# Optimization experiments

Measured on AMD Instinct MI355X. Metric: run time of the kernel, lower is better.

The kernel has to match this reference:

```python
import jax, jax.numpy as jnp
import numpy as np
from jax import lax

BETA = 10.0  # undeclared global softmax temperature in the source
STRIDE = 1
PADDING = 1


def setup_inputs() -> dict:
    key = jax.random.key(0)
    k1, k2 = jax.random.split(key)
    B, Ci, Co, K, L = 32, 256, 256, 3, 7  # num_level_conv=8 -> L=7
    x = jax.random.normal(k1, (B, Ci, 56, 56), dtype=jnp.float32)
    p_c = jax.random.normal(k2, (Co, Ci, K, K, L), dtype=jnp.float32)
    # reset_parameters with num_level=8, s=1: t1=4, t2=floor(log2(1))=0,
    # t3=arange(-2,1)=[-2,-1,0] -> q_level = sort(-2**t3) ++ [0] ++ 2**t3
    t3 = np.arange(-2, 1, dtype=np.float32)
    q_level = jnp.asarray(
        np.concatenate([np.sort(-(2.0 ** t3)), np.zeros(1, np.float32), 2.0 ** t3]),
        dtype=jnp.float32,
    )
    return {"x": x, "p_c": p_c, "q_level": q_level}


def reference(x, p_c, q_level):
    # soft quantization of the conv weight
    norm = jnp.sqrt(jnp.sum(p_c * p_c, axis=-1, keepdims=True))  # (O,I,K,K,1)
    s_c = jax.nn.softmax(BETA * (p_c / norm), axis=-1)           # (O,I,K,K,L)
    conv_w = jnp.einsum("oihwl,l->oihw", s_c, q_level)           # (O,I,K,K)
    # the source's double loop over (kh,kw) with strided slicing + matmul
    # is exactly stride-S cross-correlation with zero padding
    out = lax.conv_general_dilated(
        x,
        conv_w,
        window_strides=(STRIDE, STRIDE),
        padding=[(PADDING, PADDING), (PADDING, PADDING)],
        dimension_numbers=("NCHW", "OIHW", "NCHW"),
    )
    return out
```

## Files before the change

kernel.cpp:

```cpp
#include <hip/hip_runtime.h>
#include <math.h>

#define CI   256
#define CO   256
#define HW   56
#define LQ   7
#define BETA 10.0f

typedef __attribute__((ext_vector_type(8))) short short8;
typedef __attribute__((ext_vector_type(4))) float f32x4;

__device__ __forceinline__ ushort f2bf(float f) {
    uint u = __float_as_uint(f);
    u += 0x7FFF + ((u >> 16) & 1);
    return (ushort)(u >> 16);
}

__global__ void quant_weights(const float* __restrict__ p_c,
                              const float* __restrict__ q_level,
                              short* __restrict__ W2) {
    int idx = blockIdx.x * blockDim.x + threadIdx.x;
    if (idx >= CO * CI) return;
    int co = idx >> 8, ci = idx & 255;
    float ql[LQ];
#pragma unroll
    for (int l = 0; l < LQ; ++l) ql[l] = q_level[l];
    const float* p = p_c + (size_t)idx * 9 * LQ;
#pragma unroll
    for (int t = 0; t < 9; ++t) {
        float pv[LQ];
        float ss = 0.f;
#pragma unroll
        for (int l = 0; l < LQ; ++l) { pv[l] = p[t * LQ + l]; ss += pv[l] * pv[l]; }
        float inv = rsqrtf(ss) * BETA;
        float m = -1e30f;
#pragma unroll
        for (int l = 0; l < LQ; ++l) { pv[l] *= inv; m = fmaxf(m, pv[l]); }
        float den = 0.f, num = 0.f;
#pragma unroll
        for (int l = 0; l < LQ; ++l) {
            float e = expf(pv[l] - m);
            den += e;
            num += e * ql[l];
        }
        float val = num / den;
        int widx = ((((ci >> 5) * 9 + t) * 4 + ((ci >> 3) & 3)) * 2048) + co * 8 + (ci & 7);
        W2[widx] = (short)f2bf(val);
    }
}

__global__ void prep_border(ushort* __restrict__ xt) {
    int idx = blockIdx.x * 256 + threadIdx.x;
    int b = blockIdx.y;
    if (idx >= 228 * 32) return;
    int pos = idx >> 5, chk = idx & 31;
    int hh, ww;
    if (pos < 58)       { hh = 0;  ww = pos; }
    else if (pos < 116) { hh = 57; ww = pos - 58; }
    else { int q = pos - 116; hh = 1 + (q >> 1); ww = (q & 1) ? 57 : 0; }
    size_t o = (((size_t)b * 58 + hh) * 58 + ww) * 256 + chk * 8;
    uint4 z = {0, 0, 0, 0};
    *(uint4*)&xt[o] = z;
}

__global__ __launch_bounds__(256) void prep_main(const float* __restrict__ x,
                                                 ushort* __restrict__ xt) {
    __shared__ ushort ld[256 * 60];
    const int tid = threadIdx.x;
    const int h = blockIdx.x;
    const int b = blockIdx.y;
    const float* xp = x + ((size_t)b * CI) * 3136 + h * HW;
#pragma unroll
    for (int s = 0; s < 14; ++s) {
        int flat = s * 1024 + tid * 4;
        int ci = flat / 56;
        int w  = flat - ci * 56;
        const float4 v = *(const float4*)(xp + (size_t)ci * 3136 + w);
        ushort4 o;
        o.x = f2bf(v.x); o.y = f2bf(v.y); o.z = f2bf(v.z); o.w = f2bf(v.w);
        *(ushort4*)&ld[ci * 60 + w] = o;
    }
    __syncthreads();
    const int w = tid & 63;
    const int wq = tid >> 6;
    if (w < 56) {
        size_t obase = (((size_t)b * 58 + h + 1) * 58 + (w + 1)) * 256;
#pragma unroll
        for (int s = 0; s < 8; ++s) {
            int cig = s * 4 + wq;
            int base = (cig * 8) * 60 + w;
            uint u0 = (uint)ld[base]       | ((uint)ld[base + 60]  << 16);
            uint u1 = (uint)ld[base + 120] | ((uint)ld[base + 180] << 16);
            uint u2 = (uint)ld[base + 240] | ((uint)ld[base + 300] << 16);
            uint u3 = (uint)ld[base + 360] | ((uint)ld[base + 420] << 16);
            uint4 o = {u0, u1, u2, u3};
            *(uint4*)&xt[obase + cig * 8] = o;
        }
    }
}

__global__ __launch_bounds__(256, 2) void conv_mfma2(const ushort* __restrict__ xt_g,
                                                     const short* __restrict__ W2,
                                                     float* __restrict__ out) {
    __shared__ __align__(16) ushort xt[2][12672];

    const int tid  = threadIdx.x;
    const int lane = tid & 63;
    const int wv   = tid >> 6;
    const int l15  = lane & 15;
    const int kb   = lane >> 4;
    const int wm    = (wv >> 1) * 64;
    const int wnrow = (wv & 1) * 2;

    const int h0  = blockIdx.x * 4;
    const int co0 = blockIdx.y * 128;
    const int b   = blockIdx.z;

    int src_off[7];
#pragma unroll
    for (int s = 0; s < 7; ++s) {
        int gl = s * 64 + lane;
        int gg = wv * 396 + (gl < 396 ? gl : 0);
        int kbq = gg & 3, pos = gg >> 2;
        int r = pos / 66, c = pos - r * 66;
        int wp = c < 58 ? c : 57;
        int ci = (kbq ^ ((c >> 1) & 3)) << 3;
        src_off[s] = ((b * 58 + h0 + r) * 58 + wp) * 256 + ci;
    }

    f32x4 acc[4][8];
#pragma unroll
    for (int a = 0; a < 4; ++a)
#pragma unroll
        for (int f = 0; f < 8; ++f) acc[a][f] = (f32x4){0.f, 0.f, 0.f, 0.f};

    {
        const ushort* sp = xt_g;
        ushort* lb = &xt[0][wv * 396 * 8];
#pragma unroll
        for (int s = 0; s < 7; ++s) {
            if (s * 64 + lane < 396)
                __builtin_amdgcn_global_load_lds(
                    (const __attribute__((address_space(1))) void*)(sp + src_off[s]),
                    (__attribute__((address_space(3))) void*)(lb + s * 512), 16, 0, 0);
        }
    }

    for (int ch = 0; ch < 8; ++ch) {
        if (ch < 7) {
            const ushort* sp = xt_g + (ch + 1) * 32;
            ushort* lb = &xt[(ch + 1) & 1][wv * 396 * 8];
#pragma unroll
            for (int s = 0; s < 7; ++s) {
                if (s * 64 + lane < 396)
                    __builtin_amdgcn_global_load_lds(
                        (const __attribute__((address_space(1))) void*)(sp + src_off[s]),
                        (__attribute__((address_space(3))) void*)(lb + s * 512), 16, 0, 0);
            }
            asm volatile("s_waitcnt vmcnt(7)" ::: "memory");
        } else {
            asm volatile("s_waitcnt vmcnt(0)" ::: "memory");
        }
        __builtin_amdgcn_s_barrier();

        const ushort* buf = xt[ch & 1];
#pragma unroll
        for (int kh = 0; kh < 3; ++kh) {
#pragma unroll
            for (int kw = 0; kw < 3; ++kw) {
                const int t = kh * 3 + kw;
                const short* ap = W2 + (size_t)(((ch * 9 + t) * 4 + kb) * 256 + co0 + wm + l15) * 8;
                short8 af[4];
#pragma unroll
                for (int a = 0; a < 4; ++a) af[a] = *(const short8*)(ap + a * 128);

                const int c0 = kw + l15;
                const int r0 = wnrow + kh;
                const ushort* bp = &buf[((r0 * 66 + c0) * 4 + (kb ^ ((c0 >> 1) & 3))) * 8];
                short8 bf[8];
#pragma unroll
                for (int f = 0; f < 8; ++f)
                    bf[f] = *(const short8*)(bp + (f >> 2) * 2112 + (f & 3) * 512);

#pragma unroll
                for (int a = 0; a < 4; ++a)
#pragma unroll
                    for (int f = 0; f < 8; ++f)
                        acc[a][f] = __builtin_amdgcn_mfma_f32_16x16x32_bf16(af[a], bf[f], acc[a][f], 0, 0, 0);
            }
        }
        asm volatile("s_waitcnt lgkmcnt(0)" ::: "memory");
        __builtin_amdgcn_s_barrier();
    }

#pragma unroll
    for (int a = 0; a < 4; ++a) {
#pragma unroll
        for (int f = 0; f < 8; ++f) {
            int wloc = (f & 3) * 16 + l15;
            if (wloc < HW) {
                int h = h0 + wnrow + (f >> 2);
#pragma unroll
                for (int j = 0; j < 4; ++j) {
                    int cog = co0 + wm + 16 * a + kb * 4 + j;
                    out[(((size_t)b * CO + cog) * HW + h) * HW + wloc] = acc[a][f][j];
                }
            }
        }
    }
}

__global__ __launch_bounds__(256, 2) void conv_mfma_fb(const float* __restrict__ x,
                                                       const short* __restrict__ W2,
                                                       float* __restrict__ out) {
    __shared__ __align__(16) short xs[6 * 72 * 32];

    const int tid  = threadIdx.x;
    const int lane = tid & 63;
    const int wv   = tid >> 6;
    const int l15  = lane & 15;
    const int kb   = lane >> 4;
    const int wm    = (wv >> 1) * 64;
    const int wnrow = (wv & 1) * 2;

    const int h0  = blockIdx.x * 4;
    const int co0 = blockIdx.y * 128;
    const int b   = blockIdx.z;

    f32x4 acc[4][8];
#pragma unroll
    for (int a = 0; a < 4; ++a)
#pragma unroll
        for (int f = 0; f < 8; ++f) acc[a][f] = (f32x4){0.f, 0.f, 0.f, 0.f};

    const float* xb = x + (size_t)b * CI * HW * HW;

    for (int ch = 0; ch < 8; ++ch) {
        const int ci0 = ch * 32;
        for (int f = tid; f < 6 * 66; f += 256) {
            int r = f / 66, c = f % 66;
            int h = h0 - 1 + r, wc = c - 1;
            bool valid = (h >= 0) & (h < HW) & (wc >= 0) & (wc < HW);
            const float* xsrc = xb + (size_t)ci0 * 3136 + (valid ? (h * HW + wc) : 0);
            int sw = (c >> 1) & 3;
            int sbase = (r * 72 + c) * 32;
#pragma unroll
            for (int k = 0; k < 4; ++k) {
                short8 pk;
#pragma unroll
                for (int e = 0; e < 8; ++e) {
                    float v = xsrc[(size_t)(k * 8 + e) * 3136];
                    pk[e] = (short)f2bf(valid ? v : 0.f);
                }
                *(short8*)&xs[sbase + ((k ^ sw) * 8)] = pk;
            }
        }
        __syncthreads();

#pragma unroll
        for (int kh = 0; kh < 3; ++kh) {
#pragma unroll
            for (int kw = 0; kw < 3; ++kw) {
                const int t = kh * 3 + kw;
                const short* ap = W2 + (size_t)((((ch * 9 + t) * 4 + kb) * 256) + co0 + wm + l15) * 8;
                short8 af[4];
#pragma unroll
                for (int a = 0; a < 4; ++a) af[a] = *(const short8*)(ap + a * 128);

                const int c0 = kw + l15;
                const int r0 = wnrow + kh;
                const short* bp = &xs[(r0 * 72 + c0) * 32 + ((kb ^ ((c0 >> 1) & 3)) * 8)];
                short8 bf[8];
#pragma unroll
                for (int f = 0; f < 8; ++f)
                    bf[f] = *(const short8*)(bp + (f >> 2) * 2304 + (f & 3) * 512);

#pragma unroll
                for (int a = 0; a < 4; ++a)
#pragma unroll
                    for (int f = 0; f < 8; ++f)
                        acc[a][f] = __builtin_amdgcn_mfma_f32_16x16x32_bf16(af[a], bf[f], acc[a][f], 0, 0, 0);
            }
        }
        __syncthreads();
    }

#pragma unroll
    for (int a = 0; a < 4; ++a) {
#pragma unroll
        for (int f = 0; f < 8; ++f) {
            int wloc = (f & 3) * 16 + l15;
            if (wloc < HW) {
                int h = h0 + wnrow + (f >> 2);
#pragma unroll
                for (int j = 0; j < 4; ++j) {
                    int cog = co0 + wm + 16 * a + kb * 4 + j;
                    out[(((size_t)b * CO + cog) * HW + h) * HW + wloc] = acc[a][f][j];
                }
            }
        }
    }
}

extern "C" void kernel_launch(void* const* d_in, const int* in_sizes, int n_in,
                              void* d_out, int out_size, void* d_ws, size_t ws_size,
                              hipStream_t stream) {
    const float* x       = (const float*)d_in[0];
    const float* p_c     = (const float*)d_in[1];
    const float* q_level = (const float*)d_in[2];
    float* out = (float*)d_out;

    short* W2 = (short*)d_ws;
    const size_t XT_OFF = 2u * 1024 * 1024;
    const size_t need = XT_OFF + (size_t)32 * 3364 * 256 * 2;

    quant_weights<<<(CO * CI + 255) / 256, 256, 0, stream>>>(p_c, q_level, W2);

    if (ws_size >= need) {
        ushort* xt_g = (ushort*)((char*)d_ws + XT_OFF);
        prep_border<<<dim3(29, 32), 256, 0, stream>>>(xt_g);
        prep_main<<<dim3(56, 32), 256, 0, stream>>>(x, xt_g);
        conv_mfma2<<<dim3(14, 2, 32), 256, 0, stream>>>(xt_g, W2, out);
    } else {
        conv_mfma_fb<<<dim3(14, 2, 32), 256, 0, stream>>>(x, W2, out);
    }
}
```

Measured before the change: 181.4 us.

## Switch conv to 32x32x16 MFMA with smaller tiles, fuse border prep, parallelize quant

The main conv kernel now uses 32x32x16 bf16 MFMA instructions with a 2-row output tile per block instead of 4. This shrinks the LDS buffer and raises the occupancy target from 2 to 3 blocks and doubles the grid. Border zeroing is folded into prep_main, which removes one launch. quant_weights now uses one thread per (co,ci,tap) for more parallelism. The trade-off is less reuse of weight loads per block and more global traffic for the halo rows.

```diff
diff --git a/kernel.cpp b/kernel.cpp
--- a/kernel.cpp
+++ b/kernel.cpp
@@ -7,8 +7,9 @@
 #define LQ   7
 #define BETA 10.0f
 
-typedef __attribute__((ext_vector_type(8))) short short8;
-typedef __attribute__((ext_vector_type(4))) float f32x4;
+typedef __attribute__((ext_vector_type(8)))  short short8;
+typedef __attribute__((ext_vector_type(16))) float f32x16;
+typedef __attribute__((ext_vector_type(4)))  float f32x4;
 
 __device__ __forceinline__ ushort f2bf(float f) {
     uint u = __float_as_uint(f);
@@ -16,51 +17,32 @@
     return (ushort)(u >> 16);
 }
 
-__global__ void quant_weights(const float* __restrict__ p_c,
-                              const float* __restrict__ q_level,
-                              short* __restrict__ W2) {
-    int idx = blockIdx.x * blockDim.x + threadIdx.x;
-    if (idx >= CO * CI) return;
-    int co = idx >> 8, ci = idx & 255;
-    float ql[LQ];
-#pragma unroll
-    for (int l = 0; l < LQ; ++l) ql[l] = q_level[l];
-    const float* p = p_c + (size_t)idx * 9 * LQ;
-#pragma unroll
-    for (int t = 0; t < 9; ++t) {
-        float pv[LQ];
-        float ss = 0.f;
-#pragma unroll
-        for (int l = 0; l < LQ; ++l) { pv[l] = p[t * LQ + l]; ss += pv[l] * pv[l]; }
-        float inv = rsqrtf(ss) * BETA;
-        float m = -1e30f;
-#pragma unroll
-        for (int l = 0; l < LQ; ++l) { pv[l] *= inv; m = fmaxf(m, pv[l]); }
-        float den = 0.f, num = 0.f;
-#pragma unroll
-        for (int l = 0; l < LQ; ++l) {
-            float e = expf(pv[l] - m);
-            den += e;
-            num += e * ql[l];
-        }
-        float val = num / den;
-        int widx = ((((ci >> 5) * 9 + t) * 4 + ((ci >> 3) & 3)) * 2048) + co * 8 + (ci & 7);
-        W2[widx] = (short)f2bf(val);
-    }
-}
-
-__global__ void prep_border(ushort* __restrict__ xt) {
+__global__ __launch_bounds__(256) void quant_weights(const float* __restrict__ p_c,
+                                                     const float* __restrict__ q_level,
+                                                     short* __restrict__ W2) {
     int idx = blockIdx.x * 256 + threadIdx.x;
-    int b = blockIdx.y;
-    if (idx >= 228 * 32) return;
-    int pos = idx >> 5, chk = idx & 31;
-    int hh, ww;
-    if (pos < 58)       { hh = 0;  ww = pos; }
-    else if (pos < 116) { hh = 57; ww = pos - 58; }
-    else { int q = pos - 116; hh = 1 + (q >> 1); ww = (q & 1) ? 57 : 0; }
-    size_t o = (((size_t)b * 58 + hh) * 58 + ww) * 256 + chk * 8;
-    uint4 z = {0, 0, 0, 0};
-    *(uint4*)&xt[o] = z;
+    if (idx >= CO * CI * 9) return;
+    int coci = idx / 9;
+    int t = idx - coci * 9;
+    int co = coci >> 8, ci = coci & 255;
+    const float* p = p_c + (size_t)idx * LQ;
+    float pv[LQ];
+    float ss = 0.f;
+#pragma unroll
+    for (int l = 0; l < LQ; ++l) { pv[l] = p[l]; ss += pv[l] * pv[l]; }
+    float inv = rsqrtf(ss) * BETA;
+    float m = -1e30f;
+#pragma unroll
+    for (int l = 0; l < LQ; ++l) { pv[l] *= inv; m = fmaxf(m, pv[l]); }
+    float den = 0.f, num = 0.f;
+#pragma unroll
+    for (int l = 0; l < LQ; ++l) {
+        float e = expf(pv[l] - m);
+        den += e;
+        num += e * q_level[l];
+    }
+    int widx = ((((ci >> 5) * 9 + t) * 4 + ((ci >> 3) & 3)) * 2048) + co * 8 + (ci & 7);
+    W2[widx] = (short)f2bf(num / den);
 }
 
 __global__ __launch_bounds__(256) void prep_main(const float* __restrict__ x,
@@ -69,6 +51,22 @@
     const int tid = threadIdx.x;
     const int h = blockIdx.x;
     const int b = blockIdx.y;
+
+    if (h == 0 || h == 55) {
+        int rr = (h == 0) ? 0 : 57;
+        size_t base = ((size_t)b * 58 + rr) * 58 * 256;
+        uint4 z = {0, 0, 0, 0};
+        for (int i = tid; i < 58 * 256 / 8; i += 256)
+            *(uint4*)&xt[base + (size_t)i * 8] = z;
+    }
+    if (tid < 64) {
+        int col = (tid >> 5) * 57;
+        int chk = tid & 31;
+        size_t o = (((size_t)b * 58 + h + 1) * 58 + col) * 256 + chk * 8;
+        uint4 z = {0, 0, 0, 0};
+        *(uint4*)&xt[o] = z;
+    }
+
     const float* xp = x + ((size_t)b * CI) * 3136 + h * HW;
 #pragma unroll
     for (int s = 0; s < 14; ++s) {
@@ -99,65 +97,64 @@
     }
 }
 
-__global__ __launch_bounds__(256, 2) void conv_mfma2(const ushort* __restrict__ xt_g,
+__global__ __launch_bounds__(256, 3) void conv_mfma3(const ushort* __restrict__ xt_g,
                                                      const short* __restrict__ W2,
                                                      float* __restrict__ out) {
-    __shared__ __align__(16) ushort xt[2][12672];
+    __shared__ __align__(16) ushort xt[2][8448];
 
     const int tid  = threadIdx.x;
     const int lane = tid & 63;
     const int wv   = tid >> 6;
-    const int l15  = lane & 15;
-    const int kb   = lane >> 4;
-    const int wm    = (wv >> 1) * 64;
-    const int wnrow = (wv & 1) * 2;
-
-    const int h0  = blockIdx.x * 4;
+    const int l31  = lane & 31;
+    const int hi   = lane >> 5;
+    const int wm   = (wv >> 1) * 64;
+    const int wn   = wv & 1;
+
+    const int h0  = blockIdx.x * 2;
     const int co0 = blockIdx.y * 128;
     const int b   = blockIdx.z;
 
-    int src_off[7];
-#pragma unroll
-    for (int s = 0; s < 7; ++s) {
+    int src_off[5];
+#pragma unroll
+    for (int s = 0; s < 5; ++s) {
         int gl = s * 64 + lane;
-        int gg = wv * 396 + (gl < 396 ? gl : 0);
-        int kbq = gg & 3, pos = gg >> 2;
+        int g  = wv * 264 + (gl < 264 ? gl : 0);
+        int kbq = g & 3, pos = g >> 2;
         int r = pos / 66, c = pos - r * 66;
-        int wp = c < 58 ? c : 57;
-        int ci = (kbq ^ ((c >> 1) & 3)) << 3;
-        src_off[s] = ((b * 58 + h0 + r) * 58 + wp) * 256 + ci;
-    }
-
-    f32x4 acc[4][8];
-#pragma unroll
-    for (int a = 0; a < 4; ++a)
-#pragma unroll
-        for (int f = 0; f < 8; ++f) acc[a][f] = (f32x4){0.f, 0.f, 0.f, 0.f};
-
-    {
-        const ushort* sp = xt_g;
-        ushort* lb = &xt[0][wv * 396 * 8];
-#pragma unroll
-        for (int s = 0; s < 7; ++s) {
-            if (s * 64 + lane < 396)
-                __builtin_amdgcn_global_load_lds(
-                    (const __attribute__((address_space(1))) void*)(sp + src_off[s]),
-                    (__attribute__((address_space(3))) void*)(lb + s * 512), 16, 0, 0);
-        }
+        int cc = c < 58 ? c : 57;
+        int cig = kbq ^ ((c >> 1) & 3);
+        src_off[s] = ((b * 58 + h0 + r) * 58 + cc) * 256 + cig * 8;
+    }
+
+    f32x16 acc[2][2];
+#pragma unroll
+    for (int a = 0; a < 2; ++a)
+#pragma unroll
+        for (int f = 0; f < 2; ++f)
+#pragma unroll
+            for (int j = 0; j < 16; ++j) acc[a][f][j] = 0.f;
+
+#pragma unroll
+    for (int s = 0; s < 5; ++s) {
+        if (s * 64 + lane < 264)
+            __builtin_amdgcn_global_load_lds(
+                (const __attribute__((address_space(1))) void*)(xt_g + src_off[s]),
+                (__attribute__((address_space(3))) void*)&xt[0][(wv * 264 + s * 64) * 8],
+                16, 0, 0);
     }
 
     for (int ch = 0; ch < 8; ++ch) {
         if (ch < 7) {
             const ushort* sp = xt_g + (ch + 1) * 32;
-            ushort* lb = &xt[(ch + 1) & 1][wv * 396 * 8];
-#pragma unroll
-            for (int s = 0; s < 7; ++s) {
-                if (s * 64 + lane < 396)
+#pragma unroll
+            for (int s = 0; s < 5; ++s) {
+                if (s * 64 + lane < 264)
                     __builtin_amdgcn_global_load_lds(
                         (const __attribute__((address_space(1))) void*)(sp + src_off[s]),
-                        (__attribute__((address_space(3))) void*)(lb + s * 512), 16, 0, 0);
-            }
-            asm volatile("s_waitcnt vmcnt(7)" ::: "memory");
+                        (__attribute__((address_space(3))) void*)&xt[(ch + 1) & 1][(wv * 264 + s * 64) * 8],
+                        16, 0, 0);
+            }
+            asm volatile("s_waitcnt vmcnt(5)" ::: "memory");
         } else {
             asm volatile("s_waitcnt vmcnt(0)" ::: "memory");
         }
@@ -169,41 +166,41 @@
 #pragma unroll
             for (int kw = 0; kw < 3; ++kw) {
                 const int t = kh * 3 + kw;
-                const short* ap = W2 + (size_t)(((ch * 9 + t) * 4 + kb) * 256 + co0 + wm + l15) * 8;
-                short8 af[4];
-#pragma unroll
-                for (int a = 0; a < 4; ++a) af[a] = *(const short8*)(ap + a * 128);
-
-                const int c0 = kw + l15;
-                const int r0 = wnrow + kh;
-                const ushort* bp = &buf[((r0 * 66 + c0) * 4 + (kb ^ ((c0 >> 1) & 3))) * 8];
-                short8 bf[8];
-#pragma unroll
-                for (int f = 0; f < 8; ++f)
-                    bf[f] = *(const short8*)(bp + (f >> 2) * 2112 + (f & 3) * 512);
-
-#pragma unroll
-                for (int a = 0; a < 4; ++a)
-#pragma unroll
-                    for (int f = 0; f < 8; ++f)
-                        acc[a][f] = __builtin_amdgcn_mfma_f32_16x16x32_bf16(af[a], bf[f], acc[a][f], 0, 0, 0);
+#pragma unroll
+                for (int k2 = 0; k2 < 2; ++k2) {
+                    const int kb = k2 * 2 + hi;
+                    const short* ap = W2 + (size_t)(((ch * 9 + t) * 4 + kb) * 256 + co0 + wm + l31) * 8;
+                    short8 a0 = *(const short8*)ap;
+                    short8 a1 = *(const short8*)(ap + 32 * 8);
+
+                    const int c  = kw + l31;
+                    const int r  = wn + kh;
+                    const ushort* bp = &buf[((r * 66 + c) * 4 + (kb ^ ((c >> 1) & 3))) * 8];
+                    short8 b0 = *(const short8*)bp;
+                    short8 b1 = *(const short8*)(bp + 32 * 4 * 8);
+
+                    acc[0][0] = __builtin_amdgcn_mfma_f32_32x32x16_bf16(a0, b0, acc[0][0], 0, 0, 0);
+                    acc[0][1] = __builtin_amdgcn_mfma_f32_32x32x16_bf16(a0, b1, acc[0][1], 0, 0, 0);
+                    acc[1][0] = __builtin_amdgcn_mfma_f32_32x32x16_bf16(a1, b0, acc[1][0], 0, 0, 0);
+                    acc[1][1] = __builtin_amdgcn_mfma_f32_32x32x16_bf16(a1, b1, acc[1][1], 0, 0, 0);
+                }
             }
         }
         asm volatile("s_waitcnt lgkmcnt(0)" ::: "memory");
         __builtin_amdgcn_s_barrier();
     }
 
-#pragma unroll
-    for (int a = 0; a < 4; ++a) {
-#pragma unroll
-        for (int f = 0; f < 8; ++f) {
-            int wloc = (f & 3) * 16 + l15;
-            if (wloc < HW) {
-                int h = h0 + wnrow + (f >> 2);
-#pragma unroll
-                for (int j = 0; j < 4; ++j) {
-                    int cog = co0 + wm + 16 * a + kb * 4 + j;
-                    out[(((size_t)b * CO + cog) * HW + h) * HW + wloc] = acc[a][f][j];
+    const int h = h0 + wn;
+#pragma unroll
+    for (int a = 0; a < 2; ++a) {
+#pragma unroll
+        for (int f = 0; f < 2; ++f) {
+            int w = f * 32 + l31;
+            if (w < HW) {
+#pragma unroll
+                for (int j = 0; j < 16; ++j) {
+                    int co = co0 + wm + a * 32 + (j & 3) + 8 * (j >> 2) + 4 * hi;
+                    out[(((size_t)b * CO + co) * HW + h) * HW + w] = acc[a][f][j];
                 }
             }
         }
@@ -314,13 +311,12 @@
     const size_t XT_OFF = 2u * 1024 * 1024;
     const size_t need = XT_OFF + (size_t)32 * 3364 * 256 * 2;
 
-    quant_weights<<<(CO * CI + 255) / 256, 256, 0, stream>>>(p_c, q_level, W2);
+    quant_weights<<<(CO * CI * 9 + 255) / 256, 256, 0, stream>>>(p_c, q_level, W2);
 
     if (ws_size >= need) {
         ushort* xt_g = (ushort*)((char*)d_ws + XT_OFF);
-        prep_border<<<dim3(29, 32), 256, 0, stream>>>(xt_g);
         prep_main<<<dim3(56, 32), 256, 0, stream>>>(x, xt_g);
-        conv_mfma2<<<dim3(14, 2, 32), 256, 0, stream>>>(xt_g, W2, out);
+        conv_mfma3<<<dim3(28, 2, 32), 256, 0, stream>>>(xt_g, W2, out);
     } else {
         conv_mfma_fb<<<dim3(14, 2, 32), 256, 0, stream>>>(x, W2, out);
     }
```

Result: slower. 196.7 us (+8.4%).
